# Kernel tuning notes

Hardware: AMD Instinct MI355X
Metric: run time of the kernel (lower is better)

Reference implementation:

```python
import jax, jax.numpy as jnp
import numpy as np

N = 50000
E = 800000
F_IN, F_HID, F_OUT = 128, 128, 64


def setup_inputs() -> dict:
    key = jax.random.key(0)
    ks = jax.random.split(key, 8)
    x = jax.random.normal(ks[0], (N, F_IN), dtype=jnp.float32)
    attn_edge_index = jax.random.randint(ks[1], (2, E), 0, N, dtype=jnp.int64)
    attn_edge_weight = jax.random.uniform(ks[2], (E,), dtype=jnp.float32)
    # GCNConv params (glorot-ish scale); PyG lin has no bias, conv bias added after aggregation
    W1 = jax.random.normal(ks[3], (F_IN, F_HID), dtype=jnp.float32) * (1.0 / np.sqrt(F_IN))
    b1 = jnp.zeros((F_HID,), dtype=jnp.float32)
    W2 = jax.random.normal(ks[4], (F_HID, F_OUT), dtype=jnp.float32) * (1.0 / np.sqrt(F_HID))
    b2 = jnp.zeros((F_OUT,), dtype=jnp.float32)
    return {"x": x, "attn_edge_index": attn_edge_index, "attn_edge_weight": attn_edge_weight,
            "W1": W1, "b1": b1, "W2": W2, "b2": b2}


def _gcn_norm(edge_index, edge_weight, num_nodes):
    # Add self-loops with weight 1 (PyG gcn_norm default)
    loop = jnp.arange(num_nodes, dtype=edge_index.dtype)
    src = jnp.concatenate([edge_index[0], loop])
    dst = jnp.concatenate([edge_index[1], loop])
    w = jnp.concatenate([edge_weight, jnp.ones((num_nodes,), edge_weight.dtype)])
    deg = jax.ops.segment_sum(w, dst, num_segments=num_nodes)  # in-degree weighted
    dinv = jnp.where(deg > 0, jax.lax.rsqrt(deg), 0.0)
    norm = dinv[src] * w * dinv[dst]  # symmetric normalization
    return src, dst, norm


def _gcn_conv(h, src, dst, norm, W, b, num_nodes):
    h = h @ W                                   # [N, Fout] dense transform
    msg = norm[:, None] * h[src]                # [E+N, Fout] gather-multiply
    out = jax.ops.segment_sum(msg, dst, num_segments=num_nodes)  # scatter-add
    return out + b


def reference(x, attn_edge_index, attn_edge_weight, W1, b1, W2, b2):
    num_nodes = x.shape[0]
    src, dst, norm = _gcn_norm(attn_edge_index, attn_edge_weight, num_nodes)
    h = _gcn_conv(x, src, dst, norm, W1, b1, num_nodes)
    h = jax.nn.relu(h)
    # dropout(p=0.5) is identity in eval mode
    h = _gcn_conv(h, src, dst, norm, W2, b2, num_nodes)
    return h
```

## Files before the change

kernel.cpp:

```cpp
#include <hip/hip_runtime.h>
#include <hip/hip_bf16.h>

static constexpr int FIN   = 128;
static constexpr int FHID  = 128;
static constexpr int FOUTC = 64;
static constexpr int CAP   = 48;

typedef short bf16x8 __attribute__((ext_vector_type(8)));
typedef float f32x4 __attribute__((ext_vector_type(4)));

__device__ __forceinline__ float bfbits2f(unsigned short u) {
  union { unsigned i; float f; } c; c.i = ((unsigned)u) << 16; return c.f;
}
__device__ __forceinline__ void unpack_bf2(unsigned u, float& lo, float& hi) {
  union { unsigned i; float f; } a, b;
  a.i = u << 16;
  b.i = u & 0xffff0000u;
  lo = a.f; hi = b.f;
}
__device__ __forceinline__ unsigned short f2bfbits(float f) {
  union { float fv; unsigned i; } c; c.fv = f;
  unsigned i = c.i;
  unsigned r = i + 0x7FFFu + ((i >> 16) & 1u);
  if ((i & 0x7F800000u) == 0x7F800000u) r = i;
  return (unsigned short)(r >> 16);
}
__device__ __forceinline__ int ld_idx(const void* ei, int is64, long long off) {
  return is64 ? (int)((const long long*)ei)[off] : ((const int*)ei)[off];
}
__device__ __forceinline__ float ld_f(const void* p, int isbf, long long i) {
  return isbf ? bfbits2f(((const unsigned short*)p)[i]) : ((const float*)p)[i];
}

__global__ void setup_kernel(const unsigned short* __restrict__ xb,
                             const unsigned* __restrict__ eiw, int* __restrict__ flags,
                             int* __restrict__ cnt, int n) {
  int i = blockIdx.x * 256 + threadIdx.x;
  if (i < n) cnt[i] = 0;
  if (i == 0) {
    int isbf = 1;
    for (int k = 0; k < 256; ++k) {
      unsigned e = (xb[2 * k] >> 7) & 0xFFu;
      if (e >= 0xC0u) { isbf = 0; break; }
    }
    int is64 = 1;
    for (int k = 0; k < 64; ++k)
      if (eiw[2 * k + 1] != 0u) { is64 = 0; break; }
    flags[0] = isbf;
    flags[1] = is64;
  }
}

__global__ void fill_ell(const void* __restrict__ ei, const void* __restrict__ ew,
                         const int* __restrict__ flg, int* __restrict__ cnt,
                         int* __restrict__ ell_src, float* __restrict__ ell_w, int E) {
  int e = blockIdx.x * 256 + threadIdx.x;
  if (e >= E) return;
  int is64 = flg[1];
  int s = ld_idx(ei, is64, e);
  int d = ld_idx(ei, is64, (long long)E + e);
  float w = ld_f(ew, flg[0], e);
  int p = atomicAdd(&cnt[d], 1);
  if (p < CAP) {
    ell_src[d * CAP + p] = s;
    ell_w[d * CAP + p] = w;
  }
}

__global__ void node_dinv(int* __restrict__ cnt, const float* __restrict__ ell_w,
                          float* __restrict__ dinv, int n) {
  int i = blockIdx.x * 256 + threadIdx.x;
  if (i >= n) return;
  int c = cnt[i];
  if (c > CAP) { c = CAP; cnt[i] = CAP; }
  const float* wr = ell_w + (size_t)i * CAP;
  float s = 1.0f;
  for (int j = 0; j < c; ++j) s += wr[j];
  dinv[i] = rsqrtf(s);
}

__global__ void norm_fix(const int* __restrict__ cnt, const int* __restrict__ ell_src,
                         const float* __restrict__ dinv, float* __restrict__ ell_w, int n) {
  int gid = blockIdx.x * 256 + threadIdx.x;
  if (gid >= n * CAP) return;
  int node = gid / CAP;
  int slot = gid - node * CAP;
  if (slot < cnt[node]) ell_w[gid] *= dinv[ell_src[gid]];
}

__global__ void transpose_w(const void* __restrict__ W1, const void* __restrict__ W2,
                            const int* __restrict__ flg, unsigned short* __restrict__ Wt1,
                            unsigned short* __restrict__ Wt2) {
  int i = blockIdx.x * 256 + threadIdx.x;
  int f = flg[0];
  if (i < 128 * 128) {
    int k = i >> 7, n = i & 127;
    Wt1[n * 128 + k] = f2bfbits(ld_f(W1, f, i));
  } else {
    int j = i - 128 * 128;
    int k = j >> 6, n = j & 63;
    Wt2[n * 128 + k] = f2bfbits(ld_f(W2, f, j));
  }
}

__launch_bounds__(256)
__global__ void gather_l1(const void* __restrict__ x, const int* __restrict__ flg,
                          const int* __restrict__ cnt, const int* __restrict__ ell_src,
                          const float* __restrict__ ell_w, const float* __restrict__ dinv,
                          unsigned* __restrict__ agg, int n) {
  int wid = (blockIdx.x * 256 + threadIdx.x) >> 6;
  int lane = threadIdx.x & 63;
  if (wid >= n) return;
  int st = wid * CAP, e = st + cnt[wid];
  float a0 = 0.f, a1 = 0.f;
  float di = dinv[wid];
  float l, h;
  if (flg[0]) {
    const unsigned* xb = (const unsigned*)x;
    int j = st;
    for (; j + 4 <= e; j += 4) {
      int s0 = ell_src[j], s1 = ell_src[j + 1], s2 = ell_src[j + 2], s3 = ell_src[j + 3];
      float w0 = ell_w[j], w1 = ell_w[j + 1], w2 = ell_w[j + 2], w3 = ell_w[j + 3];
      unsigned u0 = xb[(size_t)s0 * 64 + lane];
      unsigned u1 = xb[(size_t)s1 * 64 + lane];
      unsigned u2 = xb[(size_t)s2 * 64 + lane];
      unsigned u3 = xb[(size_t)s3 * 64 + lane];
      unpack_bf2(u0, l, h); a0 = fmaf(w0, l, a0); a1 = fmaf(w0, h, a1);
      unpack_bf2(u1, l, h); a0 = fmaf(w1, l, a0); a1 = fmaf(w1, h, a1);
      unpack_bf2(u2, l, h); a0 = fmaf(w2, l, a0); a1 = fmaf(w2, h, a1);
      unpack_bf2(u3, l, h); a0 = fmaf(w3, l, a0); a1 = fmaf(w3, h, a1);
    }
    for (; j < e; ++j) {
      float w0 = ell_w[j];
      unpack_bf2(xb[(size_t)ell_src[j] * 64 + lane], l, h);
      a0 = fmaf(w0, l, a0); a1 = fmaf(w0, h, a1);
    }
    unpack_bf2(xb[(size_t)wid * 64 + lane], l, h);
  } else {
    const float2* xf = (const float2*)x;
    int j = st;
    for (; j + 4 <= e; j += 4) {
      int s0 = ell_src[j], s1 = ell_src[j + 1], s2 = ell_src[j + 2], s3 = ell_src[j + 3];
      float w0 = ell_w[j], w1 = ell_w[j + 1], w2 = ell_w[j + 2], w3 = ell_w[j + 3];
      float2 v0 = xf[(size_t)s0 * 64 + lane];
      float2 v1 = xf[(size_t)s1 * 64 + lane];
      float2 v2 = xf[(size_t)s2 * 64 + lane];
      float2 v3 = xf[(size_t)s3 * 64 + lane];
      a0 = fmaf(w0, v0.x, a0); a1 = fmaf(w0, v0.y, a1);
      a0 = fmaf(w1, v1.x, a0); a1 = fmaf(w1, v1.y, a1);
      a0 = fmaf(w2, v2.x, a0); a1 = fmaf(w2, v2.y, a1);
      a0 = fmaf(w3, v3.x, a0); a1 = fmaf(w3, v3.y, a1);
    }
    for (; j < e; ++j) {
      float w0 = ell_w[j];
      float2 v0 = xf[(size_t)ell_src[j] * 64 + lane];
      a0 = fmaf(w0, v0.x, a0); a1 = fmaf(w0, v0.y, a1);
    }
    float2 v = xf[(size_t)wid * 64 + lane];
    l = v.x; h = v.y;
  }
  a0 = di * a0 + di * di * l;
  a1 = di * a1 + di * di * h;
  agg[(size_t)wid * 64 + lane] =
      (unsigned)f2bfbits(a0) | ((unsigned)f2bfbits(a1) << 16);
}

__launch_bounds__(256)
__global__ void gather_l2(const unsigned short* __restrict__ hw2, const int* __restrict__ flg,
                          const int* __restrict__ cnt, const int* __restrict__ ell_src,
                          const float* __restrict__ ell_w, const float* __restrict__ dinv,
                          const void* __restrict__ b2, void* __restrict__ out, int n) {
  int wid = (blockIdx.x * 256 + threadIdx.x) >> 6;
  int lane = threadIdx.x & 63;
  if (wid >= n) return;
  int st = wid * CAP, e = st + cnt[wid];
  float a = 0.f;
  int j = st;
  for (; j + 4 <= e; j += 4) {
    int s0 = ell_src[j], s1 = ell_src[j + 1], s2 = ell_src[j + 2], s3 = ell_src[j + 3];
    float w0 = ell_w[j], w1 = ell_w[j + 1], w2 = ell_w[j + 2], w3 = ell_w[j + 3];
    float v0 = bfbits2f(hw2[(size_t)s0 * 64 + lane]);
    float v1 = bfbits2f(hw2[(size_t)s1 * 64 + lane]);
    float v2 = bfbits2f(hw2[(size_t)s2 * 64 + lane]);
    float v3 = bfbits2f(hw2[(size_t)s3 * 64 + lane]);
    a = fmaf(w0, v0, a); a = fmaf(w1, v1, a);
    a = fmaf(w2, v2, a); a = fmaf(w3, v3, a);
  }
  for (; j < e; ++j)
    a = fmaf(ell_w[j], bfbits2f(hw2[(size_t)ell_src[j] * 64 + lane]), a);
  float di = dinv[wid];
  a = di * a + di * di * bfbits2f(hw2[(size_t)wid * 64 + lane]);
  int isbf = flg[0];
  a += ld_f(b2, isbf, lane);
  if (isbf) ((unsigned short*)out)[(size_t)wid * 64 + lane] = f2bfbits(a);
  else ((float*)out)[(size_t)wid * 64 + lane] = a;
}

template <int FOUT, bool RELU>
__launch_bounds__(256)
__global__ void gemm_mfma(const unsigned short* __restrict__ A,
                          const unsigned short* __restrict__ Wt,
                          const void* __restrict__ bias, const int* __restrict__ flg,
                          unsigned short* __restrict__ C, int M) {
  constexpr int NT = FOUT / 16;
  __shared__ unsigned short As[128 * 128];
  __shared__ unsigned short Ws[FOUT * 128];
  const int tid = threadIdx.x;
  const int r0 = blockIdx.x * 128;

  for (int i = tid; i < 128 * 16; i += 256) {
    int r = i >> 4, c = i & 15;
    uint4 v = make_uint4(0u, 0u, 0u, 0u);
    if (r0 + r < M) v = *(const uint4*)(A + (size_t)(r0 + r) * 128 + c * 8);
    *(uint4*)&As[r * 128 + ((c ^ (r & 15)) << 3)] = v;
  }
  for (int i = tid; i < FOUT * 16; i += 256) {
    int r = i >> 4, c = i & 15;
    uint4 v = *(const uint4*)(Wt + (size_t)r * 128 + c * 8);
    *(uint4*)&Ws[r * 128 + ((c ^ (r & 15)) << 3)] = v;
  }
  __syncthreads();

  const int lane = tid & 63;
  const int wv = tid >> 6;
  const int ln15 = lane & 15;
  const int kq = lane >> 4;
  f32x4 acc[2][NT];
#pragma unroll
  for (int mi = 0; mi < 2; ++mi)
#pragma unroll
    for (int nt = 0; nt < NT; ++nt) acc[mi][nt] = (f32x4){0.f, 0.f, 0.f, 0.f};

#pragma unroll
  for (int kc = 0; kc < 4; ++kc) {
    int coff = (((kc * 4 + kq) ^ ln15) << 3);
    bf16x8 a0 = *(const bf16x8*)&As[((2 * wv + 0) * 16 + ln15) * 128 + coff];
    bf16x8 a1 = *(const bf16x8*)&As[((2 * wv + 1) * 16 + ln15) * 128 + coff];
#pragma unroll
    for (int nt = 0; nt < NT; ++nt) {
      bf16x8 b = *(const bf16x8*)&Ws[(nt * 16 + ln15) * 128 + coff];
      acc[0][nt] = __builtin_amdgcn_mfma_f32_16x16x32_bf16(a0, b, acc[0][nt], 0, 0, 0);
      acc[1][nt] = __builtin_amdgcn_mfma_f32_16x16x32_bf16(a1, b, acc[1][nt], 0, 0, 0);
    }
  }

  const int wbf = flg[0];
#pragma unroll
  for (int nt = 0; nt < NT; ++nt) {
    int col = nt * 16 + ln15;
    float bv = bias ? ld_f(bias, wbf, col) : 0.f;
#pragma unroll
    for (int mi = 0; mi < 2; ++mi) {
      int rbase = (2 * wv + mi) * 16 + kq * 4;
#pragma unroll
      for (int r = 0; r < 4; ++r) {
        int gr = r0 + rbase + r;
        if (gr < M) {
          float o = acc[mi][nt][r] + bv;
          if (RELU) o = fmaxf(o, 0.f);
          C[(size_t)gr * FOUT + col] = f2bfbits(o);
        }
      }
    }
  }
}

extern "C" void kernel_launch(void* const* d_in, const int* in_sizes, int n_in, void* d_out,
                              int out_size, void* d_ws, size_t ws_size, hipStream_t stream) {
  const void* x  = d_in[0];
  const void* ei = d_in[1];
  const void* ew = d_in[2];
  const void* W1 = d_in[3];
  const void* b1 = d_in[4];
  const void* W2 = d_in[5];
  const void* b2 = d_in[6];

  const int N = in_sizes[0] / FIN;
  const int E = in_sizes[1] / 2;
  const int B = 256;
  const int NB = (N + B - 1) / B;

  int* flags   = (int*)d_ws;
  int* cnt     = flags + 16;
  float* dinv  = (float*)(cnt + N);
  unsigned short* Wt1 = (unsigned short*)(dinv + N);
  unsigned short* Wt2 = Wt1 + 128 * 128;
  int* ell_src = (int*)(Wt2 + 64 * 128);
  float* ell_w = (float*)(ell_src + (size_t)N * CAP);
  unsigned short* agg1 = (unsigned short*)(ell_w + (size_t)N * CAP);
  unsigned short* H1   = agg1;
  unsigned short* hw2  = agg1 + (size_t)N * FHID;

  setup_kernel<<<NB, B, 0, stream>>>((const unsigned short*)x, (const unsigned*)ei, flags, cnt, N);
  fill_ell<<<(E + B - 1) / B, B, 0, stream>>>(ei, ew, flags, cnt, ell_src, ell_w, E);
  node_dinv<<<NB, B, 0, stream>>>(cnt, ell_w, dinv, N);
  norm_fix<<<((N * CAP) + B - 1) / B, B, 0, stream>>>(cnt, ell_src, dinv, ell_w, N);
  transpose_w<<<(128 * 128 + 128 * 64) / B, B, 0, stream>>>(W1, W2, flags, Wt1, Wt2);

  gather_l1<<<(N + 3) / 4, B, 0, stream>>>(x, flags, cnt, ell_src, ell_w, dinv,
                                           (unsigned*)agg1, N);
  gemm_mfma<FHID, true><<<(N + 127) / 128, B, 0, stream>>>(agg1, Wt1, b1, flags, H1, N);
  gemm_mfma<FOUTC, false><<<(N + 127) / 128, B, 0, stream>>>(H1, Wt2, nullptr, flags, hw2, N);
  gather_l2<<<(N + 3) / 4, B, 0, stream>>>(hw2, flags, cnt, ell_src, ell_w, dinv, b2, d_out, N);
}
```

Measured before the change: 273.5 us.

## Interleave ELL src/weight, warp-parallel neighbor loads, fuse two GEMMs

Stores each ELL entry as an interleaved (src, weight) pair and has each wave load its whole neighbor row in one coalesced read. Neighbor indices are then broadcast by shuffle, so eight gathers can be in flight at once in both gather kernels. The degree kernel becomes a one-wave-per-node shuffle reduction. The two layer GEMMs are fused into one kernel that keeps the ReLU'd hidden tile in LDS instead of writing and re-reading it through global memory, at the cost of more LDS per block (about 80KB), which may lower occupancy.

```diff
diff --git a/kernel.cpp b/kernel.cpp
--- a/kernel.cpp
+++ b/kernel.cpp
@@ -11,6 +11,12 @@
 
 __device__ __forceinline__ float bfbits2f(unsigned short u) {
   union { unsigned i; float f; } c; c.i = ((unsigned)u) << 16; return c.f;
+}
+__device__ __forceinline__ float wbits2f(unsigned u) {
+  union { unsigned i; float f; } c; c.i = u; return c.f;
+}
+__device__ __forceinline__ unsigned f2wbits(float f) {
+  union { float fv; unsigned i; } c; c.fv = f; return c.i;
 }
 __device__ __forceinline__ void unpack_bf2(unsigned u, float& lo, float& hi) {
   union { unsigned i; float f; } a, b;
@@ -53,7 +59,7 @@
 
 __global__ void fill_ell(const void* __restrict__ ei, const void* __restrict__ ew,
                          const int* __restrict__ flg, int* __restrict__ cnt,
-                         int* __restrict__ ell_src, float* __restrict__ ell_w, int E) {
+                         uint2* __restrict__ ell, int E) {
   int e = blockIdx.x * 256 + threadIdx.x;
   if (e >= E) return;
   int is64 = flg[1];
@@ -61,31 +67,36 @@
   int d = ld_idx(ei, is64, (long long)E + e);
   float w = ld_f(ew, flg[0], e);
   int p = atomicAdd(&cnt[d], 1);
-  if (p < CAP) {
-    ell_src[d * CAP + p] = s;
-    ell_w[d * CAP + p] = w;
-  }
-}
-
-__global__ void node_dinv(int* __restrict__ cnt, const float* __restrict__ ell_w,
+  if (p < CAP) ell[(size_t)d * CAP + p] = make_uint2((unsigned)s, f2wbits(w));
+}
+
+__global__ void node_dinv(int* __restrict__ cnt, const uint2* __restrict__ ell,
                           float* __restrict__ dinv, int n) {
-  int i = blockIdx.x * 256 + threadIdx.x;
-  if (i >= n) return;
-  int c = cnt[i];
-  if (c > CAP) { c = CAP; cnt[i] = CAP; }
-  const float* wr = ell_w + (size_t)i * CAP;
-  float s = 1.0f;
-  for (int j = 0; j < c; ++j) s += wr[j];
-  dinv[i] = rsqrtf(s);
-}
-
-__global__ void norm_fix(const int* __restrict__ cnt, const int* __restrict__ ell_src,
-                         const float* __restrict__ dinv, float* __restrict__ ell_w, int n) {
+  int wid = (blockIdx.x * 256 + threadIdx.x) >> 6;
+  int lane = threadIdx.x & 63;
+  if (wid >= n) return;
+  int c0 = cnt[wid];
+  int c = c0 > CAP ? CAP : c0;
+  uint2 rec = ell[(size_t)wid * CAP + (lane < CAP ? lane : CAP - 1)];
+  float w = (lane < c) ? wbits2f(rec.y) : 0.f;
+#pragma unroll
+  for (int off = 1; off < 64; off <<= 1) w += __shfl_xor(w, off);
+  if (lane == 0) {
+    if (c0 > CAP) cnt[wid] = CAP;
+    dinv[wid] = rsqrtf(1.f + w);
+  }
+}
+
+__global__ void norm_fix(const int* __restrict__ cnt, uint2* __restrict__ ell,
+                         const float* __restrict__ dinv, int n) {
   int gid = blockIdx.x * 256 + threadIdx.x;
   if (gid >= n * CAP) return;
   int node = gid / CAP;
   int slot = gid - node * CAP;
-  if (slot < cnt[node]) ell_w[gid] *= dinv[ell_src[gid]];
+  if (slot < cnt[node]) {
+    uint2 v = ell[gid];
+    ((unsigned*)ell)[2 * gid + 1] = f2wbits(wbits2f(v.y) * dinv[v.x]);
+  }
 }
 
 __global__ void transpose_w(const void* __restrict__ W1, const void* __restrict__ W2,
@@ -105,89 +116,110 @@
 
 __launch_bounds__(256)
 __global__ void gather_l1(const void* __restrict__ x, const int* __restrict__ flg,
-                          const int* __restrict__ cnt, const int* __restrict__ ell_src,
-                          const float* __restrict__ ell_w, const float* __restrict__ dinv,
-                          unsigned* __restrict__ agg, int n) {
+                          const int* __restrict__ cnt, const uint2* __restrict__ ell,
+                          const float* __restrict__ dinv, unsigned* __restrict__ agg, int n) {
   int wid = (blockIdx.x * 256 + threadIdx.x) >> 6;
   int lane = threadIdx.x & 63;
   if (wid >= n) return;
-  int st = wid * CAP, e = st + cnt[wid];
+  int c = cnt[wid];
+  uint2 rec = ell[(size_t)wid * CAP + (lane < CAP ? lane : CAP - 1)];
+  int rsrc = (int)rec.x;
+  float rw = wbits2f(rec.y);
   float a0 = 0.f, a1 = 0.f;
   float di = dinv[wid];
   float l, h;
+  int iters = (c + 7) >> 3;
   if (flg[0]) {
     const unsigned* xb = (const unsigned*)x;
-    int j = st;
-    for (; j + 4 <= e; j += 4) {
-      int s0 = ell_src[j], s1 = ell_src[j + 1], s2 = ell_src[j + 2], s3 = ell_src[j + 3];
-      float w0 = ell_w[j], w1 = ell_w[j + 1], w2 = ell_w[j + 2], w3 = ell_w[j + 3];
-      unsigned u0 = xb[(size_t)s0 * 64 + lane];
-      unsigned u1 = xb[(size_t)s1 * 64 + lane];
-      unsigned u2 = xb[(size_t)s2 * 64 + lane];
-      unsigned u3 = xb[(size_t)s3 * 64 + lane];
-      unpack_bf2(u0, l, h); a0 = fmaf(w0, l, a0); a1 = fmaf(w0, h, a1);
-      unpack_bf2(u1, l, h); a0 = fmaf(w1, l, a0); a1 = fmaf(w1, h, a1);
-      unpack_bf2(u2, l, h); a0 = fmaf(w2, l, a0); a1 = fmaf(w2, h, a1);
-      unpack_bf2(u3, l, h); a0 = fmaf(w3, l, a0); a1 = fmaf(w3, h, a1);
-    }
-    for (; j < e; ++j) {
-      float w0 = ell_w[j];
-      unpack_bf2(xb[(size_t)ell_src[j] * 64 + lane], l, h);
-      a0 = fmaf(w0, l, a0); a1 = fmaf(w0, h, a1);
+    for (int it = 0; it < iters; ++it) {
+      int j = it * 8;
+      int sa[8];
+      float wa[8];
+      unsigned ua[8];
+#pragma unroll
+      for (int t = 0; t < 8; ++t) {
+        int idx = j + t;
+        bool v = idx < c;
+        int sl = v ? idx : 0;
+        sa[t] = __shfl(rsrc, sl);
+        float ww = __shfl(rw, sl);
+        wa[t] = v ? ww : 0.f;
+      }
+#pragma unroll
+      for (int t = 0; t < 8; ++t) ua[t] = xb[(size_t)sa[t] * 64 + lane];
+#pragma unroll
+      for (int t = 0; t < 8; ++t) {
+        unpack_bf2(ua[t], l, h);
+        a0 = fmaf(wa[t], l, a0);
+        a1 = fmaf(wa[t], h, a1);
+      }
     }
     unpack_bf2(xb[(size_t)wid * 64 + lane], l, h);
   } else {
     const float2* xf = (const float2*)x;
-    int j = st;
-    for (; j + 4 <= e; j += 4) {
-      int s0 = ell_src[j], s1 = ell_src[j + 1], s2 = ell_src[j + 2], s3 = ell_src[j + 3];
-      float w0 = ell_w[j], w1 = ell_w[j + 1], w2 = ell_w[j + 2], w3 = ell_w[j + 3];
-      float2 v0 = xf[(size_t)s0 * 64 + lane];
-      float2 v1 = xf[(size_t)s1 * 64 + lane];
-      float2 v2 = xf[(size_t)s2 * 64 + lane];
-      float2 v3 = xf[(size_t)s3 * 64 + lane];
-      a0 = fmaf(w0, v0.x, a0); a1 = fmaf(w0, v0.y, a1);
-      a0 = fmaf(w1, v1.x, a0); a1 = fmaf(w1, v1.y, a1);
-      a0 = fmaf(w2, v2.x, a0); a1 = fmaf(w2, v2.y, a1);
-      a0 = fmaf(w3, v3.x, a0); a1 = fmaf(w3, v3.y, a1);
-    }
-    for (; j < e; ++j) {
-      float w0 = ell_w[j];
-      float2 v0 = xf[(size_t)ell_src[j] * 64 + lane];
-      a0 = fmaf(w0, v0.x, a0); a1 = fmaf(w0, v0.y, a1);
+    for (int it = 0; it < iters; ++it) {
+      int j = it * 8;
+      int sa[8];
+      float wa[8];
+      float2 va[8];
+#pragma unroll
+      for (int t = 0; t < 8; ++t) {
+        int idx = j + t;
+        bool v = idx < c;
+        int sl = v ? idx : 0;
+        sa[t] = __shfl(rsrc, sl);
+        float ww = __shfl(rw, sl);
+        wa[t] = v ? ww : 0.f;
+      }
+#pragma unroll
+      for (int t = 0; t < 8; ++t) va[t] = xf[(size_t)sa[t] * 64 + lane];
+#pragma unroll
+      for (int t = 0; t < 8; ++t) {
+        a0 = fmaf(wa[t], va[t].x, a0);
+        a1 = fmaf(wa[t], va[t].y, a1);
+      }
     }
     float2 v = xf[(size_t)wid * 64 + lane];
     l = v.x; h = v.y;
   }
   a0 = di * a0 + di * di * l;
   a1 = di * a1 + di * di * h;
-  agg[(size_t)wid * 64 + lane] =
-      (unsigned)f2bfbits(a0) | ((unsigned)f2bfbits(a1) << 16);
+  agg[(size_t)wid * 64 + lane] = (unsigned)f2bfbits(a0) | ((unsigned)f2bfbits(a1) << 16);
 }
 
 __launch_bounds__(256)
 __global__ void gather_l2(const unsigned short* __restrict__ hw2, const int* __restrict__ flg,
-                          const int* __restrict__ cnt, const int* __restrict__ ell_src,
-                          const float* __restrict__ ell_w, const float* __restrict__ dinv,
-                          const void* __restrict__ b2, void* __restrict__ out, int n) {
+                          const int* __restrict__ cnt, const uint2* __restrict__ ell,
+                          const float* __restrict__ dinv, const void* __restrict__ b2,
+                          void* __restrict__ out, int n) {
   int wid = (blockIdx.x * 256 + threadIdx.x) >> 6;
   int lane = threadIdx.x & 63;
   if (wid >= n) return;
-  int st = wid * CAP, e = st + cnt[wid];
+  int c = cnt[wid];
+  uint2 rec = ell[(size_t)wid * CAP + (lane < CAP ? lane : CAP - 1)];
+  int rsrc = (int)rec.x;
+  float rw = wbits2f(rec.y);
   float a = 0.f;
-  int j = st;
-  for (; j + 4 <= e; j += 4) {
-    int s0 = ell_src[j], s1 = ell_src[j + 1], s2 = ell_src[j + 2], s3 = ell_src[j + 3];
-    float w0 = ell_w[j], w1 = ell_w[j + 1], w2 = ell_w[j + 2], w3 = ell_w[j + 3];
-    float v0 = bfbits2f(hw2[(size_t)s0 * 64 + lane]);
-    float v1 = bfbits2f(hw2[(size_t)s1 * 64 + lane]);
-    float v2 = bfbits2f(hw2[(size_t)s2 * 64 + lane]);
-    float v3 = bfbits2f(hw2[(size_t)s3 * 64 + lane]);
-    a = fmaf(w0, v0, a); a = fmaf(w1, v1, a);
-    a = fmaf(w2, v2, a); a = fmaf(w3, v3, a);
-  }
-  for (; j < e; ++j)
-    a = fmaf(ell_w[j], bfbits2f(hw2[(size_t)ell_src[j] * 64 + lane]), a);
+  int iters = (c + 7) >> 3;
+  for (int it = 0; it < iters; ++it) {
+    int j = it * 8;
+    int sa[8];
+    float wa[8];
+    unsigned short va[8];
+#pragma unroll
+    for (int t = 0; t < 8; ++t) {
+      int idx = j + t;
+      bool v = idx < c;
+      int sl = v ? idx : 0;
+      sa[t] = __shfl(rsrc, sl);
+      float ww = __shfl(rw, sl);
+      wa[t] = v ? ww : 0.f;
+    }
+#pragma unroll
+    for (int t = 0; t < 8; ++t) va[t] = hw2[(size_t)sa[t] * 64 + lane];
+#pragma unroll
+    for (int t = 0; t < 8; ++t) a = fmaf(wa[t], bfbits2f(va[t]), a);
+  }
   float di = dinv[wid];
   a = di * a + di * di * bfbits2f(hw2[(size_t)wid * 64 + lane]);
   int isbf = flg[0];
@@ -196,28 +228,33 @@
   else ((float*)out)[(size_t)wid * 64 + lane] = a;
 }
 
-template <int FOUT, bool RELU>
 __launch_bounds__(256)
-__global__ void gemm_mfma(const unsigned short* __restrict__ A,
-                          const unsigned short* __restrict__ Wt,
-                          const void* __restrict__ bias, const int* __restrict__ flg,
-                          unsigned short* __restrict__ C, int M) {
-  constexpr int NT = FOUT / 16;
+__global__ void gemm12(const unsigned short* __restrict__ agg1,
+                       const unsigned short* __restrict__ Wt1,
+                       const unsigned short* __restrict__ Wt2,
+                       const void* __restrict__ b1, const int* __restrict__ flg,
+                       unsigned short* __restrict__ hw2, int M) {
   __shared__ unsigned short As[128 * 128];
-  __shared__ unsigned short Ws[FOUT * 128];
+  __shared__ unsigned short W1s[128 * 128];
+  __shared__ unsigned short W2s[64 * 128];
   const int tid = threadIdx.x;
   const int r0 = blockIdx.x * 128;
 
   for (int i = tid; i < 128 * 16; i += 256) {
-    int r = i >> 4, c = i & 15;
+    int r = i >> 4, ch = i & 15;
     uint4 v = make_uint4(0u, 0u, 0u, 0u);
-    if (r0 + r < M) v = *(const uint4*)(A + (size_t)(r0 + r) * 128 + c * 8);
-    *(uint4*)&As[r * 128 + ((c ^ (r & 15)) << 3)] = v;
-  }
-  for (int i = tid; i < FOUT * 16; i += 256) {
-    int r = i >> 4, c = i & 15;
-    uint4 v = *(const uint4*)(Wt + (size_t)r * 128 + c * 8);
-    *(uint4*)&Ws[r * 128 + ((c ^ (r & 15)) << 3)] = v;
+    if (r0 + r < M) v = *(const uint4*)(agg1 + (size_t)(r0 + r) * 128 + ch * 8);
+    *(uint4*)&As[r * 128 + ((ch ^ (r & 15)) << 3)] = v;
+  }
+  for (int i = tid; i < 128 * 16; i += 256) {
+    int r = i >> 4, ch = i & 15;
+    uint4 v = *(const uint4*)(Wt1 + (size_t)r * 128 + ch * 8);
+    *(uint4*)&W1s[r * 128 + ((ch ^ (r & 15)) << 3)] = v;
+  }
+  for (int i = tid; i < 64 * 16; i += 256) {
+    int r = i >> 4, ch = i & 15;
+    uint4 v = *(const uint4*)(Wt2 + (size_t)r * 128 + ch * 8);
+    *(uint4*)&W2s[r * 128 + ((ch ^ (r & 15)) << 3)] = v;
   }
   __syncthreads();
 
@@ -225,41 +262,68 @@
   const int wv = tid >> 6;
   const int ln15 = lane & 15;
   const int kq = lane >> 4;
-  f32x4 acc[2][NT];
+  const int wbf = flg[0];
+
+  f32x4 acc1[2][8];
 #pragma unroll
   for (int mi = 0; mi < 2; ++mi)
 #pragma unroll
-    for (int nt = 0; nt < NT; ++nt) acc[mi][nt] = (f32x4){0.f, 0.f, 0.f, 0.f};
-
+    for (int nt = 0; nt < 8; ++nt) acc1[mi][nt] = (f32x4){0.f, 0.f, 0.f, 0.f};
 #pragma unroll
   for (int kc = 0; kc < 4; ++kc) {
     int coff = (((kc * 4 + kq) ^ ln15) << 3);
     bf16x8 a0 = *(const bf16x8*)&As[((2 * wv + 0) * 16 + ln15) * 128 + coff];
     bf16x8 a1 = *(const bf16x8*)&As[((2 * wv + 1) * 16 + ln15) * 128 + coff];
 #pragma unroll
-    for (int nt = 0; nt < NT; ++nt) {
-      bf16x8 b = *(const bf16x8*)&Ws[(nt * 16 + ln15) * 128 + coff];
-      acc[0][nt] = __builtin_amdgcn_mfma_f32_16x16x32_bf16(a0, b, acc[0][nt], 0, 0, 0);
-      acc[1][nt] = __builtin_amdgcn_mfma_f32_16x16x32_bf16(a1, b, acc[1][nt], 0, 0, 0);
-    }
-  }
-
-  const int wbf = flg[0];
-#pragma unroll
-  for (int nt = 0; nt < NT; ++nt) {
+    for (int nt = 0; nt < 8; ++nt) {
+      bf16x8 b = *(const bf16x8*)&W1s[(nt * 16 + ln15) * 128 + coff];
+      acc1[0][nt] = __builtin_amdgcn_mfma_f32_16x16x32_bf16(a0, b, acc1[0][nt], 0, 0, 0);
+      acc1[1][nt] = __builtin_amdgcn_mfma_f32_16x16x32_bf16(a1, b, acc1[1][nt], 0, 0, 0);
+    }
+  }
+
+#pragma unroll
+  for (int nt = 0; nt < 8; ++nt) {
     int col = nt * 16 + ln15;
-    float bv = bias ? ld_f(bias, wbf, col) : 0.f;
+    float bv = ld_f(b1, wbf, col);
 #pragma unroll
     for (int mi = 0; mi < 2; ++mi) {
-      int rbase = (2 * wv + mi) * 16 + kq * 4;
 #pragma unroll
       for (int r = 0; r < 4; ++r) {
-        int gr = r0 + rbase + r;
-        if (gr < M) {
-          float o = acc[mi][nt][r] + bv;
-          if (RELU) o = fmaxf(o, 0.f);
-          C[(size_t)gr * FOUT + col] = f2bfbits(o);
-        }
+        int row = 32 * wv + mi * 16 + kq * 4 + r;
+        float o = fmaxf(acc1[mi][nt][r] + bv, 0.f);
+        As[row * 128 + ((((col >> 3)) ^ (row & 15)) << 3) + (col & 7)] = f2bfbits(o);
+      }
+    }
+  }
+  __syncthreads();
+
+  f32x4 acc2[2][4];
+#pragma unroll
+  for (int mi = 0; mi < 2; ++mi)
+#pragma unroll
+    for (int nt = 0; nt < 4; ++nt) acc2[mi][nt] = (f32x4){0.f, 0.f, 0.f, 0.f};
+#pragma unroll
+  for (int kc = 0; kc < 4; ++kc) {
+    int coff = (((kc * 4 + kq) ^ ln15) << 3);
+    bf16x8 a0 = *(const bf16x8*)&As[((2 * wv + 0) * 16 + ln15) * 128 + coff];
+    bf16x8 a1 = *(const bf16x8*)&As[((2 * wv + 1) * 16 + ln15) * 128 + coff];
+#pragma unroll
+    for (int nt = 0; nt < 4; ++nt) {
+      bf16x8 b = *(const bf16x8*)&W2s[(nt * 16 + ln15) * 128 + coff];
+      acc2[0][nt] = __builtin_amdgcn_mfma_f32_16x16x32_bf16(a0, b, acc2[0][nt], 0, 0, 0);
+      acc2[1][nt] = __builtin_amdgcn_mfma_f32_16x16x32_bf16(a1, b, acc2[1][nt], 0, 0, 0);
+    }
+  }
+#pragma unroll
+  for (int nt = 0; nt < 4; ++nt) {
+    int col = nt * 16 + ln15;
+#pragma unroll
+    for (int mi = 0; mi < 2; ++mi) {
+#pragma unroll
+      for (int r = 0; r < 4; ++r) {
+        int gr = r0 + 32 * wv + mi * 16 + kq * 4 + r;
+        if (gr < M) hw2[(size_t)gr * 64 + col] = f2bfbits(acc2[mi][nt][r]);
       }
     }
   }
@@ -285,21 +349,17 @@
   float* dinv  = (float*)(cnt + N);
   unsigned short* Wt1 = (unsigned short*)(dinv + N);
   unsigned short* Wt2 = Wt1 + 128 * 128;
-  int* ell_src = (int*)(Wt2 + 64 * 128);
-  float* ell_w = (float*)(ell_src + (size_t)N * CAP);
-  unsigned short* agg1 = (unsigned short*)(ell_w + (size_t)N * CAP);
-  unsigned short* H1   = agg1;
+  uint2* ell   = (uint2*)(Wt2 + 64 * 128);
+  unsigned short* agg1 = (unsigned short*)(ell + (size_t)N * CAP);
   unsigned short* hw2  = agg1 + (size_t)N * FHID;
 
   setup_kernel<<<NB, B, 0, stream>>>((const unsigned short*)x, (const unsigned*)ei, flags, cnt, N);
-  fill_ell<<<(E + B - 1) / B, B, 0, stream>>>(ei, ew, flags, cnt, ell_src, ell_w, E);
-  node_dinv<<<NB, B, 0, stream>>>(cnt, ell_w, dinv, N);
-  norm_fix<<<((N * CAP) + B - 1) / B, B, 0, stream>>>(cnt, ell_src, dinv, ell_w, N);
   transpose_w<<<(128 * 128 + 128 * 64) / B, B, 0, stream>>>(W1, W2, flags, Wt1, Wt2);
-
-  gather_l1<<<(N + 3) / 4, B, 0, stream>>>(x, flags, cnt, ell_src, ell_w, dinv,
-                                           (unsigned*)agg1, N);
-  gemm_mfma<FHID, true><<<(N + 127) / 128, B, 0, stream>>>(agg1, Wt1, b1, flags, H1, N);
-  gemm_mfma<FOUTC, false><<<(N + 127) / 128, B, 0, stream>>>(H1, Wt2, nullptr, flags, hw2, N);
-  gather_l2<<<(N + 3) / 4, B, 0, stream>>>(hw2, flags, cnt, ell_src, ell_w, dinv, b2, d_out, N);
-}
+  fill_ell<<<(E + B - 1) / B, B, 0, stream>>>(ei, ew, flags, cnt, ell, E);
+  node_dinv<<<(N + 3) / 4, B, 0, stream>>>(cnt, ell, dinv, N);
+  norm_fix<<<((N * CAP) + B - 1) / B, B, 0, stream>>>(cnt, ell, dinv, N);
+
+  gather_l1<<<(N + 3) / 4, B, 0, stream>>>(x, flags, cnt, ell, dinv, (unsigned*)agg1, N);
+  gemm12<<<(N + 127) / 128, B, 0, stream>>>(agg1, Wt1, Wt2, b1, flags, hw2, N);
+  gather_l2<<<(N + 3) / 4, B, 0, stream>>>(hw2, flags, cnt, ell, dinv, b2, d_out, N);
+}
```

Result: faster. 246.1 us (-10.0%).
